# Performance work log

Hardware: AMD Instinct MI355X
Metric: run time of the kernel (lower is better)

## Reference

```python
import jax, jax.numpy as jnp
import numpy as np
import math

NUM_HEADS = 16
ROPE_BASE = 10000.0
SLIDING_WINDOW = 512  # note: original triu-then-tril composition makes the mask empty (no-op)


def _rope_cos_sin(seq_len, head_dim, dtype):
    inv_freq = 1.0 / (ROPE_BASE ** (jnp.arange(0, head_dim, 2, dtype=jnp.float32) / head_dim))
    t = jnp.arange(seq_len, dtype=jnp.float32)
    freqs = t[:, None] * inv_freq[None, :]          # [S, D/2]
    emb = jnp.concatenate([freqs, freqs], axis=-1)  # [S, D]
    # reshape to broadcast over [B, S, H, D]
    return jnp.cos(emb)[None, :, None, :].astype(dtype), jnp.sin(emb)[None, :, None, :].astype(dtype)


def _rotate_half(x):
    x1, x2 = jnp.split(x, 2, axis=-1)
    return jnp.concatenate([-x2, x1], axis=-1)


def setup_inputs() -> dict:
    key = jax.random.key(0)
    ks = jax.random.split(key, 9)
    B, S, E = 2, 2048, 2048
    sc = 1.0 / math.sqrt(E)
    return {
        "hidden_states": jax.random.normal(ks[0], (B, S, E), dtype=jnp.float32),
        "Wq": jax.random.normal(ks[1], (E, E), dtype=jnp.float32) * sc,
        "bq": jax.random.normal(ks[2], (E,), dtype=jnp.float32) * 0.01,
        "Wk": jax.random.normal(ks[3], (E, E), dtype=jnp.float32) * sc,
        "bk": jax.random.normal(ks[4], (E,), dtype=jnp.float32) * 0.01,
        "Wv": jax.random.normal(ks[5], (E, E), dtype=jnp.float32) * sc,
        "bv": jax.random.normal(ks[6], (E,), dtype=jnp.float32) * 0.01,
        "Wo": jax.random.normal(ks[7], (E, E), dtype=jnp.float32) * sc,
        "bo": jax.random.normal(ks[8], (E,), dtype=jnp.float32) * 0.01,
    }


def reference(hidden_states, Wq, bq, Wk, bk, Wv, bv, Wo, bo):
    B, S, E = hidden_states.shape
    H = NUM_HEADS
    D = E // H
    q = (hidden_states @ Wq.T + bq).reshape(B, S, H, D)
    k = (hidden_states @ Wk.T + bk).reshape(B, S, H, D)
    v = (hidden_states @ Wv.T + bv).reshape(B, S, H, D)

    cos, sin = _rope_cos_sin(S, D, q.dtype)
    q = q * cos + _rotate_half(q) * sin
    k = k * cos + _rotate_half(k) * sin

    scale = 1.0 / math.sqrt(D)
    scores = jnp.einsum("bqhd,bkhd->bhqk", q, k) * scale  # [B,H,S,S]
    # Faithful to source: triu(ones, +w) followed by tril(..., -w) is empty -> mask is a no-op.
    attn = jax.nn.softmax(scores, axis=-1)
    out = jnp.einsum("bhqk,bkhd->bqhd", attn, v).reshape(B, S, E)
    return out @ Wo.T + bo
```

## Files before the change

kernel.cpp:

```cpp
#include <hip/hip_runtime.h>
#include <hip/hip_bf16.h>

#define B_ 2
#define S_ 2048
#define E_ 2048
#define H_ 16
#define D_ 128
#define M_ (B_*S_)
#define NQKV_ (3*E_)

typedef __attribute__((ext_vector_type(8))) short bf16x8;
typedef __attribute__((ext_vector_type(4))) float f32x4;
typedef __attribute__((ext_vector_type(4))) unsigned short u16x4;
typedef __attribute__((ext_vector_type(2))) unsigned u32x2;

__device__ __forceinline__ unsigned short f2bf(float f) {
  union { float f; unsigned u; } v; v.f = f;
  unsigned r = v.u + 0x7fffu + ((v.u >> 16) & 1u);
  return (unsigned short)(r >> 16);
}
__device__ __forceinline__ float bf2f(unsigned short h) {
  union { unsigned u; float f; } v; v.u = ((unsigned)h) << 16;
  return v.f;
}

__device__ __forceinline__ void gload_lds16(const void* g, void* l) {
  __builtin_amdgcn_global_load_lds(
      (const __attribute__((address_space(1))) unsigned*)g,
      (__attribute__((address_space(3))) unsigned*)l, 16, 0, 0);
}

__global__ __launch_bounds__(256) void prep_kernel(
    const float* __restrict__ hs,
    const float* __restrict__ Wq, const float* __restrict__ Wk, const float* __restrict__ Wv,
    const float* __restrict__ Wo,
    const float* __restrict__ bq, const float* __restrict__ bk, const float* __restrict__ bv,
    unsigned short* __restrict__ hsb, unsigned short* __restrict__ Wqkv,
    unsigned short* __restrict__ Wob, float* __restrict__ biasqkv,
    float* __restrict__ cosT, float* __restrict__ sinT)
{
  const int seg = blockIdx.y;
  const int t0 = blockIdx.x * 256 + threadIdx.x;
  const int stride = gridDim.x * 256;
  if (seg == 0) {
    const int n = (M_*E_)/4;
    for (int i = t0; i < n; i += stride) {
      f32x4 v = ((const f32x4*)hs)[i];
      u16x4 o; o[0]=f2bf(v[0]); o[1]=f2bf(v[1]); o[2]=f2bf(v[2]); o[3]=f2bf(v[3]);
      ((u16x4*)hsb)[i] = o;
    }
  } else if (seg == 1) {
    const int n = (3*E_*E_)/4;
    for (int i = t0; i < n; i += stride) {
      int e4 = i << 2;
      int r = e4 >> 11;
      int k = e4 & 2047;
      const float* src = (r < E_) ? (Wq + ((size_t)r << 11) + k)
                       : (r < 2*E_) ? (Wk + ((size_t)(r - E_) << 11) + k)
                       : (Wv + ((size_t)(r - 2*E_) << 11) + k);
      f32x4 v = *(const f32x4*)src;
      u16x4 o; o[0]=f2bf(v[0]); o[1]=f2bf(v[1]); o[2]=f2bf(v[2]); o[3]=f2bf(v[3]);
      ((u16x4*)Wqkv)[i] = o;
    }
  } else if (seg == 2) {
    const int n = (E_*E_)/4;
    for (int i = t0; i < n; i += stride) {
      f32x4 v = ((const f32x4*)Wo)[i];
      u16x4 o; o[0]=f2bf(v[0]); o[1]=f2bf(v[1]); o[2]=f2bf(v[2]); o[3]=f2bf(v[3]);
      ((u16x4*)Wob)[i] = o;
    }
  } else if (seg == 3) {
    for (int i = t0; i < NQKV_; i += stride)
      biasqkv[i] = (i < E_) ? bq[i] : (i < 2*E_) ? bk[i - E_] : bv[i - 2*E_];
  } else {
    for (int i = t0; i < S_*64; i += stride) {
      int j = i & 63, s = i >> 6;
      float inv = exp2f(-(float)j * (13.287712379549449f / 64.0f));
      float ang = (float)s * inv;
      cosT[i] = cosf(ang);
      sinT[i] = sinf(ang);
    }
  }
}

#define STAGE8(basePtr, BUF, AB, KS, KT) do { \
    unsigned short* dst_ = lds + (BUF)*32768 + (AB)*16384 + (KS)*8192; \
    const unsigned short* src_ = (basePtr) + (KT)*64 + (KS)*32; \
    _Pragma("unroll") \
    for (int j_ = 0; j_ < 2; ++j_) { \
      int cc_ = (j_ << 9) + tid; \
      int row_ = cc_ >> 2, c2_ = cc_ & 3; \
      int sc_ = c2_ ^ ((row_ >> 1) & 3); \
      gload_lds16(src_ + (size_t)row_*K + sc_*8, (char*)dst_ + cc_*16); \
    } } while(0)

#define LOADA8(MH, KS, BUF) do { \
    const unsigned short* Ab_ = lds + (BUF)*32768 + (KS)*8192; \
    _Pragma("unroll") \
    for (int j_ = 0; j_ < 4; ++j_) { \
      int row_ = wr*128 + ((MH)*4 + j_)*16 + l15; \
      af[j_] = *(const bf16x8*)(Ab_ + row_*32 + ((l4 ^ ((row_>>1)&3)) << 3)); \
    } } while(0)

#define LOADB8(KS, BUF) do { \
    const unsigned short* Bb_ = lds + (BUF)*32768 + 16384 + (KS)*8192; \
    _Pragma("unroll") \
    for (int j_ = 0; j_ < 4; ++j_) { \
      int row_ = wc*64 + j_*16 + l15; \
      bf[j_] = *(const bf16x8*)(Bb_ + row_*32 + ((l4 ^ ((row_>>1)&3)) << 3)); \
    } } while(0)

#define MFMAQ(MH) do { \
    _Pragma("unroll") \
    for (int mm_ = 0; mm_ < 4; ++mm_) \
      _Pragma("unroll") \
      for (int nn_ = 0; nn_ < 4; ++nn_) \
        acc[(MH)*4+mm_][nn_] = __builtin_amdgcn_mfma_f32_16x16x32_bf16(af[mm_], bf[nn_], acc[(MH)*4+mm_][nn_], 0,0,0); \
  } while(0)

#define WVM6 asm volatile("s_waitcnt vmcnt(6)" ::: "memory")
#define WVM0 asm volatile("s_waitcnt vmcnt(0)" ::: "memory")

#define PHASE(MH, KS, BUF, ISSUE, WAITV) do { \
    LOADA8(MH, KS, BUF); \
    if ((MH) == 0) LOADB8(KS, BUF); \
    ISSUE; \
    __builtin_amdgcn_sched_barrier(0); \
    __builtin_amdgcn_s_barrier(); \
    asm volatile("s_waitcnt lgkmcnt(0)" ::: "memory"); \
    __builtin_amdgcn_sched_barrier(0); \
    __builtin_amdgcn_s_setprio(1); \
    MFMAQ(MH); \
    __builtin_amdgcn_s_setprio(0); \
    WAITV; \
    __builtin_amdgcn_s_barrier(); \
  } while(0)

__global__ __launch_bounds__(512, 2) void gemm8(
    const unsigned short* __restrict__ A,
    const unsigned short* __restrict__ Bm,
    const float* __restrict__ bias,
    unsigned short* __restrict__ Cv,
    int M, int N, int K, int ldc)
{
  __shared__ __align__(16) unsigned short lds[65536];
  const int tid = threadIdx.x;
  const int lane = tid & 63;
  const int w = tid >> 6;
  const int wr = w >> 2, wc = w & 3;
  const int l15 = lane & 15, l4 = lane >> 4;

  const int ntile = N >> 8;
  int wg = blockIdx.x;
  const int cpx = gridDim.x >> 3;
  wg = (wg & 7) * cpx + (wg >> 3);
  const int tm = wg / ntile, tn = wg % ntile;

  const unsigned short* Abase = A + ((size_t)tm*256)*K;
  const unsigned short* Bbase = Bm + ((size_t)tn*256)*K;

  f32x4 acc[8][4] = {};
  bf16x8 af[4], bf[4];

  const int NITER = K >> 7;

  STAGE8(Bbase, 0, 1, 0, 0); STAGE8(Abase, 0, 0, 0, 0);
  STAGE8(Bbase, 0, 1, 1, 0); STAGE8(Abase, 0, 0, 1, 0);
  STAGE8(Bbase, 1, 1, 0, 1); STAGE8(Abase, 1, 0, 0, 1);
  STAGE8(Bbase, 1, 1, 1, 1);
  __builtin_amdgcn_sched_barrier(0);
  WVM6;
  __builtin_amdgcn_s_barrier();

  for (int i = 0; i < NITER; ++i) {
    const int t1k = 2*i + 1, t2k = 2*i + 2, t3k = 2*i + 3;
    const bool nl = (i < NITER - 1);
    PHASE(0, 0, 0, STAGE8(Abase, 1, 0, 1, t1k), );
    PHASE(1, 0, 0, if (nl) STAGE8(Bbase, 0, 1, 0, t2k), );
    PHASE(0, 1, 0, if (nl) STAGE8(Abase, 0, 0, 0, t2k), );
    PHASE(1, 1, 0, if (nl) STAGE8(Bbase, 0, 1, 1, t2k), if (nl) WVM6; else WVM0);
    PHASE(0, 0, 1, if (nl) STAGE8(Abase, 0, 0, 1, t2k), );
    PHASE(1, 0, 1, if (nl) STAGE8(Bbase, 1, 1, 0, t3k), );
    PHASE(0, 1, 1, if (nl) STAGE8(Abase, 1, 0, 0, t3k), );
    PHASE(1, 1, 1, if (nl) STAGE8(Bbase, 1, 1, 1, t3k), if (nl) WVM6);
  }

  #pragma unroll
  for (int mt = 0; mt < 8; ++mt) {
    #pragma unroll
    for (int nt = 0; nt < 4; ++nt) {
      int colg = tn*256 + wc*64 + nt*16 + l15;
      float bvv = bias[colg];
      #pragma unroll
      for (int r = 0; r < 4; ++r) {
        int rowg = tm*256 + wr*128 + mt*16 + l4*4 + r;
        Cv[(size_t)rowg*ldc + colg] = f2bf(acc[mt][nt][r] + bvv);
      }
    }
  }
}

#define STGA(BUFP, TKT, KS) do { \
    unsigned short* dst_ = lds + (BUFP)*24576 + (KS)*4096; \
    const unsigned short* src_ = Abase + (TKT)*64 + (KS)*32; \
    int cc_ = tid; int row_ = cc_ >> 2, c2_ = cc_ & 3; \
    int sc_ = c2_ ^ ((row_ >> 1) & 3); \
    gload_lds16(src_ + (size_t)row_*K + sc_*8, (char*)dst_ + cc_*16); \
  } while(0)

#define STGB(BUFP, TKT, KS) do { \
    unsigned short* dst_ = lds + (BUFP)*24576 + 8192 + (KS)*8192; \
    const unsigned short* src_ = Bbase + (TKT)*64 + (KS)*32; \
    _Pragma("unroll") \
    for (int j_ = 0; j_ < 2; ++j_) { \
      int cc_ = (j_ << 9) + tid; int row_ = cc_ >> 2, c2_ = cc_ & 3; \
      int sc_ = c2_ ^ ((row_ >> 1) & 3); \
      gload_lds16(src_ + (size_t)row_*K + sc_*8, (char*)dst_ + cc_*16); \
    } } while(0)

#define PHA(KS, BUF, ISSUE, WAITV) do { \
    { const unsigned short* Ab_ = lds + (BUF)*24576 + (KS)*4096; \
      _Pragma("unroll") \
      for (int j_ = 0; j_ < 4; ++j_) { \
        int row_ = wr*64 + j_*16 + l15; \
        af[j_] = *(const bf16x8*)(Ab_ + row_*32 + ((l4 ^ ((row_>>1)&3)) << 3)); } \
      const unsigned short* Bb_ = lds + (BUF)*24576 + 8192 + (KS)*8192; \
      _Pragma("unroll") \
      for (int j_ = 0; j_ < 4; ++j_) { \
        int row_ = wc*64 + j_*16 + l15; \
        bf[j_] = *(const bf16x8*)(Bb_ + row_*32 + ((l4 ^ ((row_>>1)&3)) << 3)); } } \
    ISSUE; \
    __builtin_amdgcn_sched_barrier(0); \
    __builtin_amdgcn_s_barrier(); \
    asm volatile("s_waitcnt lgkmcnt(0)" ::: "memory"); \
    __builtin_amdgcn_sched_barrier(0); \
    __builtin_amdgcn_s_setprio(1); \
    _Pragma("unroll") \
    for (int mm_ = 0; mm_ < 4; ++mm_) \
      _Pragma("unroll") \
      for (int nn_ = 0; nn_ < 4; ++nn_) \
        acc[mm_][nn_] = __builtin_amdgcn_mfma_f32_16x16x32_bf16(af[mm_], bf[nn_], acc[mm_][nn_], 0,0,0); \
    __builtin_amdgcn_s_setprio(0); \
    WAITV; \
    __builtin_amdgcn_s_barrier(); \
  } while(0)

template<int OUT_F32>
__global__ __launch_bounds__(512, 2) void gemmA(
    const unsigned short* __restrict__ A,
    const unsigned short* __restrict__ Bm,
    const float* __restrict__ bias,
    void* __restrict__ Cv,
    int M, int N, int K, int ldc)
{
  __shared__ __align__(16) unsigned short lds[73728];
  const int tid = threadIdx.x;
  const int lane = tid & 63;
  const int w = tid >> 6;
  const int wr = w >> 2, wc = w & 3;
  const int l15 = lane & 15, l4 = lane >> 4;

  const int ntile = N >> 8;
  int wg = blockIdx.x;
  const int cpx = gridDim.x >> 3;
  wg = (wg & 7) * cpx + (wg >> 3);
  const int tm = wg / ntile, tn = wg % ntile;

  const unsigned short* Abase = A + ((size_t)tm*128)*K;
  const unsigned short* Bbase = Bm + ((size_t)tn*256)*K;

  f32x4 acc[4][4] = {};
  bf16x8 af[4], bf[4];

  const int NT = K >> 6;

  STGA(0,0,0); STGB(0,0,0); STGA(0,0,1); STGB(0,0,1);
  STGA(1,1,0); STGB(1,1,0); STGA(1,1,1); STGB(1,1,1);
  __builtin_amdgcn_sched_barrier(0);
  asm volatile("s_waitcnt vmcnt(6)" ::: "memory");
  __builtin_amdgcn_s_barrier();
  __builtin_amdgcn_sched_barrier(0);

  int bufc = 0, bufn = 2;
  for (int i = 0; i < NT; ++i) {
    const bool st = (i + 2 < NT);
    const bool more = (i + 1 < NT);
    PHA(0, bufc, if (st) { STGA(bufn, i+2, 0); STGB(bufn, i+2, 0); }, );
    PHA(1, bufc, if (st) { STGA(bufn, i+2, 1); STGB(bufn, i+2, 1); },
        if (st) { asm volatile("s_waitcnt vmcnt(6)" ::: "memory"); }
        else if (more) { asm volatile("s_waitcnt vmcnt(0)" ::: "memory"); });
    bufc = (bufc + 1 == 3) ? 0 : bufc + 1;
    bufn = (bufn + 1 == 3) ? 0 : bufn + 1;
  }

  #pragma unroll
  for (int mt = 0; mt < 4; ++mt) {
    #pragma unroll
    for (int nt = 0; nt < 4; ++nt) {
      int colg = tn*256 + wc*64 + nt*16 + l15;
      float bvv = bias[colg];
      #pragma unroll
      for (int r = 0; r < 4; ++r) {
        int rowg = tm*128 + wr*64 + mt*16 + l4*4 + r;
        float v = acc[mt][nt][r] + bvv;
        if (OUT_F32) ((float*)Cv)[(size_t)rowg*ldc + colg] = v;
        else ((unsigned short*)Cv)[(size_t)rowg*ldc + colg] = f2bf(v);
      }
    }
  }
}

__global__ __launch_bounds__(256) void rope_kernel(
    unsigned short* __restrict__ qkv, const float* __restrict__ cosT, const float* __restrict__ sinT)
{
  int t = blockIdx.x*256 + threadIdx.x;
  int i  = t & 63;
  int h  = (t >> 6) & 15;
  int m  = t >> 10;
  int s  = m & (S_-1);
  float c = cosT[s*64 + i], sn = sinT[s*64 + i];
  const float scale = 0.08838834764831845f * 1.4426950408889634f;
  size_t base = (size_t)m*NQKV_ + h*128;
  float q1 = bf2f(qkv[base+i]), q2 = bf2f(qkv[base+64+i]);
  qkv[base+i]    = f2bf((q1*c - q2*sn)*scale);
  qkv[base+64+i] = f2bf((q2*c + q1*sn)*scale);
  size_t kb = base + E_;
  float k1 = bf2f(qkv[kb+i]), k2 = bf2f(qkv[kb+64+i]);
  qkv[kb+i]    = f2bf(k1*c - k2*sn);
  qkv[kb+64+i] = f2bf(k2*c + k1*sn);
}

__global__ __launch_bounds__(256) void transv_kernel(
    const unsigned short* __restrict__ qkv, unsigned short* __restrict__ Vt)
{
  __shared__ unsigned short t[32][33];
  int bid = blockIdx.x;
  int st = bid & 63;
  int dt = (bid >> 6) & 3;
  int bh = bid >> 8;
  int b = bh >> 4, h = bh & 15;
  int tx = threadIdx.x & 31, ty = threadIdx.x >> 5;
  #pragma unroll
  for (int j = 0; j < 4; ++j) {
    int r = ty + j*8;
    t[r][tx] = qkv[(size_t)(b*S_ + st*32 + r)*NQKV_ + 2*E_ + h*128 + dt*32 + tx];
  }
  __syncthreads();
  #pragma unroll
  for (int j = 0; j < 4; ++j) {
    int r = ty + j*8;
    Vt[((size_t)bh*D_ + dt*32 + r)*S_ + st*32 + tx] = t[tx][r];
  }
}

__global__ __launch_bounds__(256, 2) void attn_kernel(
    const unsigned short* __restrict__ qkv, const unsigned short* __restrict__ Vt,
    unsigned short* __restrict__ Ao)
{
  __shared__ unsigned short lK[64*128];
  __shared__ unsigned short lV[128*64];
  __shared__ __align__(16) unsigned short lP[4*32*64];
  int bid = blockIdx.x;
  bid = (bid & 7)*64 + (bid >> 3);
  const int qt = bid & 15;
  const int bh = bid >> 4;
  const int b = bh >> 4, h = bh & 15;
  const int tid = threadIdx.x, lane = tid & 63, w = tid >> 6;
  const int l15 = lane & 15, l4 = lane >> 4;

  bf16x8 qf[2][4];
  #pragma unroll
  for (int g = 0; g < 2; ++g) {
    const int qrow = qt*128 + w*32 + g*16 + l15;
    const unsigned short* qp = qkv + (size_t)(b*S_ + qrow)*NQKV_ + h*128 + l4*8;
    #pragma unroll
    for (int f = 0; f < 4; ++f) qf[g][f] = *(const bf16x8*)(qp + f*32);
  }

  f32x4 O[2][8];
  #pragma unroll
  for (int g = 0; g < 2; ++g)
    #pragma unroll
    for (int i = 0; i < 8; ++i) O[g][i] = (f32x4){0.f,0.f,0.f,0.f};
  float mx[2] = {-1e30f,-1e30f}, lsum[2] = {0.f,0.f};

  unsigned short* myP = lP + w*(32*64);
  const int ksw = (l15 & 7) << 3;
  const size_t kbase = (size_t)b*S_*NQKV_ + E_ + (size_t)h*128;
  const size_t vbase = (size_t)bh*D_*S_;

  for (int kt = 0; kt < S_; kt += 64) {
    #pragma unroll
    for (int i = 0; i < 4; ++i) {
      int cc = i*256 + tid;
      int row = cc >> 4, col = cc & 15;
      int scol = col ^ (row & 7);
      gload_lds16(qkv + kbase + (size_t)(kt + row)*NQKV_ + scol*8, (char*)lK + cc*16);
    }
    #pragma unroll
    for (int i = 0; i < 4; ++i) {
      int cc = i*256 + tid;
      int row = cc >> 3, col = cc & 7;
      int scol = col ^ ((row & 7) ^ ((row >> 3) & 7));
      gload_lds16(Vt + vbase + (size_t)row*S_ + kt + scol*8, (char*)lV + cc*16);
    }
    asm volatile("s_waitcnt vmcnt(0)" ::: "memory");
    __syncthreads();

    f32x4 sfr[2][4];
    #pragma unroll
    for (int nf = 0; nf < 4; ++nf) {
      f32x4 s0 = (f32x4){0.f,0.f,0.f,0.f};
      f32x4 s1 = (f32x4){0.f,0.f,0.f,0.f};
      #pragma unroll
      for (int ks = 0; ks < 4; ++ks) {
        int row = nf*16 + l15;
        int ch = (ks*4 + l4) ^ (row & 7);
        bf16x8 kf = *(const bf16x8*)(lK + row*128 + ch*8);
        s0 = __builtin_amdgcn_mfma_f32_16x16x32_bf16(kf, qf[0][ks], s0, 0, 0, 0);
        s1 = __builtin_amdgcn_mfma_f32_16x16x32_bf16(kf, qf[1][ks], s1, 0, 0, 0);
      }
      sfr[0][nf] = s0; sfr[1][nf] = s1;
    }

    float vm[2];
    #pragma unroll
    for (int g = 0; g < 2; ++g) {
      float v = -1e30f;
      #pragma unroll
      for (int nf = 0; nf < 4; ++nf)
        #pragma unroll
        for (int r = 0; r < 4; ++r) v = fmaxf(v, sfr[g][nf][r]);
      v = fmaxf(v, __shfl_xor(v, 16, 64));
      v = fmaxf(v, __shfl_xor(v, 32, 64));
      vm[g] = v;
    }

    if (__any((vm[0] > mx[0] + 8.0f) || (vm[1] > mx[1] + 8.0f))) {
      #pragma unroll
      for (int g = 0; g < 2; ++g) {
        float mn = fmaxf(mx[g], vm[g]);
        float al = __builtin_amdgcn_exp2f(mx[g] - mn);
        mx[g] = mn;
        lsum[g] *= al;
        #pragma unroll
        for (int r = 0; r < 4; ++r) {
          float ar = __shfl(al, (lane & 48) + l4*4 + r, 64);
          #pragma unroll
          for (int df = 0; df < 8; ++df) O[g][df][r] *= ar;
        }
      }
    }

    #pragma unroll
    for (int g = 0; g < 2; ++g) {
      float ps = 0.f;
      #pragma unroll
      for (int nf = 0; nf < 4; ++nf) {
        #pragma unroll
        for (int r = 0; r < 4; ++r) {
          float p = __builtin_amdgcn_exp2f(sfr[g][nf][r] - mx[g]);
          sfr[g][nf][r] = p;
          ps += p;
        }
      }
      ps += __shfl_xor(ps, 16, 64);
      ps += __shfl_xor(ps, 32, 64);
      lsum[g] += ps;
    }

    #pragma unroll
    for (int g = 0; g < 2; ++g) {
      #pragma unroll
      for (int nf = 0; nf < 4; ++nf) {
        unsigned lo = (unsigned)f2bf(sfr[g][nf][0]) | ((unsigned)f2bf(sfr[g][nf][1]) << 16);
        unsigned hi = (unsigned)f2bf(sfr[g][nf][2]) | ((unsigned)f2bf(sfr[g][nf][3]) << 16);
        int k0 = (nf*16 + l4*4) ^ ksw;
        u32x2 val; val[0] = lo; val[1] = hi;
        *(u32x2*)(myP + (g*16 + l15)*64 + k0) = val;
      }
    }
    asm volatile("s_waitcnt lgkmcnt(0)" ::: "memory");

    #pragma unroll
    for (int ks2 = 0; ks2 < 2; ++ks2) {
      int kk = (ks2*32 + l4*8) ^ ksw;
      bf16x8 pf0 = *(const bf16x8*)(myP + l15*64 + kk);
      bf16x8 pf1 = *(const bf16x8*)(myP + (16 + l15)*64 + kk);
      #pragma unroll
      for (int df = 0; df < 8; ++df) {
        int row = df*16 + l15;
        int ch = (ks2*4 + l4) ^ ((row & 7) ^ ((row >> 3) & 7));
        bf16x8 vf = *(const bf16x8*)(lV + row*64 + ch*8);
        O[0][df] = __builtin_amdgcn_mfma_f32_16x16x32_bf16(pf0, vf, O[0][df], 0, 0, 0);
        O[1][df] = __builtin_amdgcn_mfma_f32_16x16x32_bf16(pf1, vf, O[1][df], 0, 0, 0);
      }
    }
    __syncthreads();
  }

  #pragma unroll
  for (int g = 0; g < 2; ++g) {
    float linv = 1.0f / lsum[g];
    float inv[4];
    #pragma unroll
    for (int r = 0; r < 4; ++r) inv[r] = __shfl(linv, (lane & 48) + l4*4 + r, 64);
    #pragma unroll
    for (int df = 0; df < 8; ++df) {
      int colg = h*128 + df*16 + l15;
      #pragma unroll
      for (int r = 0; r < 4; ++r) {
        int rowg = qt*128 + w*32 + g*16 + l4*4 + r;
        Ao[(size_t)(b*S_ + rowg)*E_ + colg] = f2bf(O[g][df][r] * inv[r]);
      }
    }
  }
}

extern "C" void kernel_launch(void* const* d_in, const int* in_sizes, int n_in,
                              void* d_out, int out_size, void* d_ws, size_t ws_size,
                              hipStream_t stream) {
  const float* hs = (const float*)d_in[0];
  const float* Wq = (const float*)d_in[1];
  const float* bq = (const float*)d_in[2];
  const float* Wk = (const float*)d_in[3];
  const float* bk = (const float*)d_in[4];
  const float* Wv = (const float*)d_in[5];
  const float* bv = (const float*)d_in[6];
  const float* Wo = (const float*)d_in[7];
  const float* bo = (const float*)d_in[8];
  float* out = (float*)d_out;

  char* p = (char*)d_ws;
  auto alloc = [&](size_t bytes) { char* r = p; p += (bytes + 255) & ~(size_t)255; return r; };
  unsigned short* hsb  = (unsigned short*)alloc((size_t)M_*E_*2);
  unsigned short* Wqkv = (unsigned short*)alloc((size_t)NQKV_*E_*2);
  unsigned short* Wob  = (unsigned short*)alloc((size_t)E_*E_*2);
  unsigned short* qkv  = (unsigned short*)alloc((size_t)M_*NQKV_*2);
  unsigned short* Vt   = (unsigned short*)alloc((size_t)B_*H_*D_*S_*2);
  unsigned short* Ao   = (unsigned short*)alloc((size_t)M_*E_*2);
  float* biasqkv = (float*)alloc((size_t)NQKV_*4);
  float* cosT = (float*)alloc((size_t)S_*64*4);
  float* sinT = (float*)alloc((size_t)S_*64*4);

  prep_kernel<<<dim3(2048, 5), 256, 0, stream>>>(hs, Wq, Wk, Wv, Wo, bq, bk, bv,
      hsb, Wqkv, Wob, biasqkv, cosT, sinT);
  gemm8<<<dim3((M_/256)*(2*E_/256)), 512, 0, stream>>>(
      hsb, Wqkv, biasqkv, qkv, M_, 2*E_, E_, NQKV_);
  gemmA<0><<<dim3((M_/128)*(E_/256)), 512, 0, stream>>>(
      hsb, Wqkv + (size_t)2*E_*E_, biasqkv + 2*E_, qkv + 2*E_, M_, E_, E_, NQKV_);
  rope_kernel<<<dim3((M_*H_*64)/256), 256, 0, stream>>>(qkv, cosT, sinT);
  transv_kernel<<<dim3(B_*H_*(D_/32)*(S_/32)), 256, 0, stream>>>(qkv, Vt);
  attn_kernel<<<dim3(B_*H_*(S_/128)), 256, 0, stream>>>(qkv, Vt, Ao);
  gemmA<1><<<dim3((M_/128)*(E_/256)), 512, 0, stream>>>(
      Ao, Wob, bo, out, M_, E_, E_, E_);
}
```

Measured before the change: 278.9 us.

## Double-buffer K/V tiles and enlarge attention query tile to 256 rows

The attention kernel now prefetches the next K/V tile into a second LDS buffer while computing on the current one, so global loads overlap MFMA work. Each wave handles 64 query rows instead of 32, doubling K/V reuse per load and halving the grid to 256 blocks. It also raises wave priority around the MFMA phases and uses the packed bf16 convert instruction. The costs are higher register and LDS use (launch bounds drop to one block per CU) and fewer blocks, which may leave CUs underused on a 256-CU part.

```diff
diff --git a/kernel.cpp b/kernel.cpp
--- a/kernel.cpp
+++ b/kernel.cpp
@@ -353,79 +353,94 @@
   }
 }
 
-__global__ __launch_bounds__(256, 2) void attn_kernel(
+__global__ __launch_bounds__(256, 1) void attn_kernel(
     const unsigned short* __restrict__ qkv, const unsigned short* __restrict__ Vt,
     unsigned short* __restrict__ Ao)
 {
-  __shared__ unsigned short lK[64*128];
-  __shared__ unsigned short lV[128*64];
-  __shared__ __align__(16) unsigned short lP[4*32*64];
+  __shared__ unsigned short lK[2][64*128];
+  __shared__ unsigned short lV[2][128*64];
+  __shared__ __align__(16) unsigned short lP[4*64*64];
   int bid = blockIdx.x;
-  bid = (bid & 7)*64 + (bid >> 3);
-  const int qt = bid & 15;
-  const int bh = bid >> 4;
+  bid = (bid & 7)*32 + (bid >> 3);
+  const int qt = bid & 7;
+  const int bh = bid >> 3;
   const int b = bh >> 4, h = bh & 15;
   const int tid = threadIdx.x, lane = tid & 63, w = tid >> 6;
   const int l15 = lane & 15, l4 = lane >> 4;
 
-  bf16x8 qf[2][4];
-  #pragma unroll
-  for (int g = 0; g < 2; ++g) {
-    const int qrow = qt*128 + w*32 + g*16 + l15;
+  bf16x8 qf[4][4];
+  #pragma unroll
+  for (int g = 0; g < 4; ++g) {
+    const int qrow = qt*256 + w*64 + g*16 + l15;
     const unsigned short* qp = qkv + (size_t)(b*S_ + qrow)*NQKV_ + h*128 + l4*8;
     #pragma unroll
     for (int f = 0; f < 4; ++f) qf[g][f] = *(const bf16x8*)(qp + f*32);
   }
 
-  f32x4 O[2][8];
-  #pragma unroll
-  for (int g = 0; g < 2; ++g)
+  f32x4 O[4][8];
+  #pragma unroll
+  for (int g = 0; g < 4; ++g)
     #pragma unroll
     for (int i = 0; i < 8; ++i) O[g][i] = (f32x4){0.f,0.f,0.f,0.f};
-  float mx[2] = {-1e30f,-1e30f}, lsum[2] = {0.f,0.f};
-
-  unsigned short* myP = lP + w*(32*64);
+  float mx[4] = {-1e30f,-1e30f,-1e30f,-1e30f}, lsum[4] = {0.f,0.f,0.f,0.f};
+
+  unsigned short* myP = lP + w*(64*64);
   const int ksw = (l15 & 7) << 3;
   const size_t kbase = (size_t)b*S_*NQKV_ + E_ + (size_t)h*128;
   const size_t vbase = (size_t)bh*D_*S_;
 
-  for (int kt = 0; kt < S_; kt += 64) {
-    #pragma unroll
-    for (int i = 0; i < 4; ++i) {
-      int cc = i*256 + tid;
-      int row = cc >> 4, col = cc & 15;
-      int scol = col ^ (row & 7);
-      gload_lds16(qkv + kbase + (size_t)(kt + row)*NQKV_ + scol*8, (char*)lK + cc*16);
-    }
-    #pragma unroll
-    for (int i = 0; i < 4; ++i) {
-      int cc = i*256 + tid;
-      int row = cc >> 3, col = cc & 7;
-      int scol = col ^ ((row & 7) ^ ((row >> 3) & 7));
-      gload_lds16(Vt + vbase + (size_t)row*S_ + kt + scol*8, (char*)lV + cc*16);
-    }
-    asm volatile("s_waitcnt vmcnt(0)" ::: "memory");
-    __syncthreads();
-
-    f32x4 sfr[2][4];
+  #define ASTAGE(bi, ktile) do { \
+    _Pragma("unroll") \
+    for (int i_ = 0; i_ < 4; ++i_) { \
+      int cc_ = i_*256 + tid; \
+      int row_ = cc_ >> 4, col_ = cc_ & 15; \
+      int scol_ = col_ ^ (row_ & 7); \
+      gload_lds16(qkv + kbase + (size_t)((ktile)*64 + row_)*NQKV_ + scol_*8, \
+                  (char*)(&lK[bi][0]) + cc_*16); \
+    } \
+    _Pragma("unroll") \
+    for (int i_ = 0; i_ < 4; ++i_) { \
+      int cc_ = i_*256 + tid; \
+      int row_ = cc_ >> 3, col_ = cc_ & 7; \
+      int scol_ = col_ ^ ((row_ & 7) ^ ((row_ >> 3) & 7)); \
+      gload_lds16(Vt + vbase + (size_t)row_*S_ + (ktile)*64 + scol_*8, \
+                  (char*)(&lV[bi][0]) + cc_*16); \
+    } } while(0)
+
+  ASTAGE(0, 0);
+  asm volatile("s_waitcnt vmcnt(0)" ::: "memory");
+  __syncthreads();
+
+  for (int it = 0; it < S_/64; ++it) {
+    const int cur = it & 1;
+    if (it + 1 < S_/64) ASTAGE(cur ^ 1, it + 1);
+    __builtin_amdgcn_sched_barrier(0);
+
+    f32x4 sfr[4][4];
+    __builtin_amdgcn_s_setprio(1);
     #pragma unroll
     for (int nf = 0; nf < 4; ++nf) {
       f32x4 s0 = (f32x4){0.f,0.f,0.f,0.f};
       f32x4 s1 = (f32x4){0.f,0.f,0.f,0.f};
+      f32x4 s2 = (f32x4){0.f,0.f,0.f,0.f};
+      f32x4 s3 = (f32x4){0.f,0.f,0.f,0.f};
       #pragma unroll
       for (int ks = 0; ks < 4; ++ks) {
         int row = nf*16 + l15;
         int ch = (ks*4 + l4) ^ (row & 7);
-        bf16x8 kf = *(const bf16x8*)(lK + row*128 + ch*8);
+        bf16x8 kf = *(const bf16x8*)(&lK[cur][0] + row*128 + ch*8);
         s0 = __builtin_amdgcn_mfma_f32_16x16x32_bf16(kf, qf[0][ks], s0, 0, 0, 0);
         s1 = __builtin_amdgcn_mfma_f32_16x16x32_bf16(kf, qf[1][ks], s1, 0, 0, 0);
-      }
-      sfr[0][nf] = s0; sfr[1][nf] = s1;
-    }
-
-    float vm[2];
-    #pragma unroll
-    for (int g = 0; g < 2; ++g) {
+        s2 = __builtin_amdgcn_mfma_f32_16x16x32_bf16(kf, qf[2][ks], s2, 0, 0, 0);
+        s3 = __builtin_amdgcn_mfma_f32_16x16x32_bf16(kf, qf[3][ks], s3, 0, 0, 0);
+      }
+      sfr[0][nf] = s0; sfr[1][nf] = s1; sfr[2][nf] = s2; sfr[3][nf] = s3;
+    }
+    __builtin_amdgcn_s_setprio(0);
+
+    float vm[4];
+    #pragma unroll
+    for (int g = 0; g < 4; ++g) {
       float v = -1e30f;
       #pragma unroll
       for (int nf = 0; nf < 4; ++nf)
@@ -436,9 +451,10 @@
       vm[g] = v;
     }
 
-    if (__any((vm[0] > mx[0] + 8.0f) || (vm[1] > mx[1] + 8.0f))) {
-      #pragma unroll
-      for (int g = 0; g < 2; ++g) {
+    if (__any((vm[0] > mx[0] + 8.0f) || (vm[1] > mx[1] + 8.0f) ||
+              (vm[2] > mx[2] + 8.0f) || (vm[3] > mx[3] + 8.0f))) {
+      #pragma unroll
+      for (int g = 0; g < 4; ++g) {
         float mn = fmaxf(mx[g], vm[g]);
         float al = __builtin_amdgcn_exp2f(mx[g] - mn);
         mx[g] = mn;
@@ -453,7 +469,7 @@
     }
 
     #pragma unroll
-    for (int g = 0; g < 2; ++g) {
+    for (int g = 0; g < 4; ++g) {
       float ps = 0.f;
       #pragma unroll
       for (int nf = 0; nf < 4; ++nf) {
@@ -470,11 +486,12 @@
     }
 
     #pragma unroll
-    for (int g = 0; g < 2; ++g) {
+    for (int g = 0; g < 4; ++g) {
       #pragma unroll
       for (int nf = 0; nf < 4; ++nf) {
-        unsigned lo = (unsigned)f2bf(sfr[g][nf][0]) | ((unsigned)f2bf(sfr[g][nf][1]) << 16);
-        unsigned hi = (unsigned)f2bf(sfr[g][nf][2]) | ((unsigned)f2bf(sfr[g][nf][3]) << 16);
+        unsigned lo, hi;
+        asm("v_cvt_pk_bf16_f32 %0, %1, %2" : "=v"(lo) : "v"(sfr[g][nf][0]), "v"(sfr[g][nf][1]));
+        asm("v_cvt_pk_bf16_f32 %0, %1, %2" : "=v"(hi) : "v"(sfr[g][nf][2]), "v"(sfr[g][nf][3]));
         int k0 = (nf*16 + l4*4) ^ ksw;
         u32x2 val; val[0] = lo; val[1] = hi;
         *(u32x2*)(myP + (g*16 + l15)*64 + k0) = val;
@@ -482,25 +499,32 @@
     }
     asm volatile("s_waitcnt lgkmcnt(0)" ::: "memory");
 
+    __builtin_amdgcn_s_setprio(1);
     #pragma unroll
     for (int ks2 = 0; ks2 < 2; ++ks2) {
       int kk = (ks2*32 + l4*8) ^ ksw;
       bf16x8 pf0 = *(const bf16x8*)(myP + l15*64 + kk);
       bf16x8 pf1 = *(const bf16x8*)(myP + (16 + l15)*64 + kk);
+      bf16x8 pf2 = *(const bf16x8*)(myP + (32 + l15)*64 + kk);
+      bf16x8 pf3 = *(const bf16x8*)(myP + (48 + l15)*64 + kk);
       #pragma unroll
       for (int df = 0; df < 8; ++df) {
         int row = df*16 + l15;
         int ch = (ks2*4 + l4) ^ ((row & 7) ^ ((row >> 3) & 7));
-        bf16x8 vf = *(const bf16x8*)(lV + row*64 + ch*8);
+        bf16x8 vf = *(const bf16x8*)(&lV[cur][0] + row*64 + ch*8);
         O[0][df] = __builtin_amdgcn_mfma_f32_16x16x32_bf16(pf0, vf, O[0][df], 0, 0, 0);
         O[1][df] = __builtin_amdgcn_mfma_f32_16x16x32_bf16(pf1, vf, O[1][df], 0, 0, 0);
-      }
-    }
+        O[2][df] = __builtin_amdgcn_mfma_f32_16x16x32_bf16(pf2, vf, O[2][df], 0, 0, 0);
+        O[3][df] = __builtin_amdgcn_mfma_f32_16x16x32_bf16(pf3, vf, O[3][df], 0, 0, 0);
+      }
+    }
+    __builtin_amdgcn_s_setprio(0);
+    asm volatile("s_waitcnt vmcnt(0)" ::: "memory");
     __syncthreads();
   }
 
   #pragma unroll
-  for (int g = 0; g < 2; ++g) {
+  for (int g = 0; g < 4; ++g) {
     float linv = 1.0f / lsum[g];
     float inv[4];
     #pragma unroll
@@ -510,7 +534,7 @@
       int colg = h*128 + df*16 + l15;
       #pragma unroll
       for (int r = 0; r < 4; ++r) {
-        int rowg = qt*128 + w*32 + g*16 + l4*4 + r;
+        int rowg = qt*256 + w*64 + g*16 + l4*4 + r;
         Ao[(size_t)(b*S_ + rowg)*E_ + colg] = f2bf(O[g][df][r] * inv[r]);
       }
     }
@@ -551,7 +575,7 @@
       hsb, Wqkv + (size_t)2*E_*E_, biasqkv + 2*E_, qkv + 2*E_, M_, E_, E_, NQKV_);
   rope_kernel<<<dim3((M_*H_*64)/256), 256, 0, stream>>>(qkv, cosT, sinT);
   transv_kernel<<<dim3(B_*H_*(D_/32)*(S_/32)), 256, 0, stream>>>(qkv, Vt);
-  attn_kernel<<<dim3(B_*H_*(S_/128)), 256, 0, stream>>>(qkv, Vt, Ao);
+  attn_kernel<<<dim3(B_*H_*(S_/256)), 256, 0, stream>>>(qkv, Vt, Ao);
   gemmA<1><<<dim3((M_/128)*(E_/256)), 512, 0, stream>>>(
       Ao, Wob, bo, out, M_, E_, E_, E_);
 }
```

After: 338.1 us. 1.21x slower.
